# Performance work log

Hardware: AMD Instinct MI355X
Metric: run time of the kernel (lower is better)

The kernel has to match this reference:

```python
import jax, jax.numpy as jnp
import numpy as np

NU, NI, E = 20000, 8000, 64
DV, DT = 4096, 768
NE, B = 200000, 4096
L_HET, L_HOMO = 2, 1
K_ISG, K_UCG = 10, 20
MMW, WD = 0.1, 1e-4


def setup_inputs() -> dict:
    ks = jax.random.split(jax.random.key(0), 14)
    return {
        "feat_v": jax.random.normal(ks[0], (NI, DV), jnp.float32),
        "feat_t": jax.random.normal(ks[1], (NI, DT), jnp.float32),
        "pref_v": jax.random.normal(ks[2], (NU, E), jnp.float32) * 0.1,
        "pref_t": jax.random.normal(ks[3], (NU, E), jnp.float32) * 0.1,
        "W_v": jax.random.normal(ks[4], (DV, E), jnp.float32) * 0.02,
        "W_t": jax.random.normal(ks[5], (DT, E), jnp.float32) * 0.02,
        "user_v_alpha": jax.random.normal(ks[6], (1,), jnp.float32),
        "user_nb_weights": jax.random.normal(ks[7], (NU, K_UCG), jnp.float32),
        "edge_users": jax.random.randint(ks[8], (NE,), 0, NU, jnp.int32),
        "edge_items": jax.random.randint(ks[9], (NE,), 0, NI, jnp.int32),
        "u_ids": jax.random.randint(ks[10], (B,), 0, NU, jnp.int32),
        "pos_ids": jax.random.randint(ks[11], (B,), 0, NI, jnp.int32),
        "neg_ids": jax.random.randint(ks[12], (B,), 0, NI, jnp.int32),
        "user_nb": jax.random.randint(ks[13], (NU, K_UCG), 0, NU, jnp.int32),
    }


def reference(feat_v, feat_t, pref_v, pref_t, W_v, W_t, user_v_alpha,
              user_nb_weights, edge_users, edge_items, u_ids, pos_ids,
              neg_ids, user_nb):
    N = NU + NI
    # bidirectional bipartite edges (items offset by NU)
    src = jnp.concatenate([edge_users, edge_items + NU])
    dst = jnp.concatenate([edge_items + NU, edge_users])
    deg = jax.ops.segment_sum(jnp.ones_like(src, jnp.float32), dst, num_segments=N)
    deg = jnp.maximum(deg, 1.0)
    norm = (1.0 / jnp.sqrt(deg[src] * deg[dst]))[:, None]

    def hetero_gcn(feat, pref, W):
        x = jnp.concatenate([pref, feat @ W], axis=0)  # [N, E]
        h, out = x, x
        for _ in range(L_HET):
            h = jax.ops.segment_sum(h[src] * norm, dst, num_segments=N)
            out = out + h
        return out[:NU], out[NU:]

    u_v, i_v = hetero_gcn(feat_v, pref_v, W_v)
    u_t, i_t = hetero_gcn(feat_t, pref_t, W_t)
    a_v = jax.nn.sigmoid(user_v_alpha[0])
    u_f = jnp.concatenate([a_v * u_v, (1.0 - a_v) * u_t], axis=1)  # [NU, 2E]
    i_f = jnp.concatenate([i_v, i_t], axis=1)                      # [NI, 2E]

    # Item Semantic Graph: KNN over cosine sim, no grad through adjacency.
    def knn_adj(f):
        fn = f / jnp.linalg.norm(f, axis=-1, keepdims=True)
        sim = fn @ fn.T                       # [NI, NI]
        _, idx = jax.lax.top_k(sim, K_ISG)
        return jnp.zeros((NI, NI), f.dtype).at[jnp.arange(NI)[:, None], idx].set(1.0)

    adj = jax.lax.stop_gradient(MMW * knn_adj(feat_v) + (1.0 - MMW) * knn_adj(feat_t))
    rs = adj.sum(axis=1)
    adj = adj * jnp.where(rs > 0, 1.0 / rs, 0.0)[:, None]

    h_i = i_f
    for _ in range(L_HOMO):
        h_i = adj @ h_i

    # User Co-occurrence Graph: scatter-softmax attention aggregation, vectorized.
    attn = jax.nn.softmax(user_nb_weights, axis=1)  # [NU, K]
    h_u = u_f
    for _ in range(L_HOMO):
        h_u = jnp.einsum('uk,ukd->ud', attn, h_u[user_nb])

    z_u = u_f + h_u
    z_i = i_f + h_i
    pos = jnp.sum(z_u[u_ids] * z_i[pos_ids], axis=1)
    neg = jnp.sum(z_u[u_ids] * z_i[neg_ids], axis=1)
    bpr = -jnp.mean(jax.nn.log_sigmoid(pos - neg))
    reg = WD * (jnp.sum(pref_v ** 2) + jnp.sum(pref_t ** 2) + user_v_alpha[0] ** 2) / 2.0
    return bpr + reg
```

## Files before the change

kernel.cpp:

```cpp
#include <hip/hip_runtime.h>
#include <cstdint>
#include <cstddef>

#define NU_C   20000
#define NI_C   8000
#define NTOT_C 28000
#define NE_C   200000
#define B_C    4096
#define NPAD_C 8064
#define NCHUNK 63
#define NPAIR  2016
#define NEB    782

typedef unsigned short u16;
typedef unsigned int   u32;
typedef unsigned char  u8;
typedef __bf16 bf16x8 __attribute__((ext_vector_type(8)));
typedef float  f32x4  __attribute__((ext_vector_type(4)));

static __device__ __forceinline__ u16 f2bf(float f) {
  u32 u = __float_as_uint(f);
  return (u16)((u + 0x7fffu + ((u >> 16) & 1u)) >> 16);
}

static __device__ __forceinline__ void gl_lds16(const void* g, void* l) {
  __builtin_amdgcn_global_load_lds(
      (const __attribute__((address_space(1))) void*)g,
      (__attribute__((address_space(3))) void*)l, 16, 0, 0);
}

static __device__ __forceinline__ int xcd_swz(int b) {
  return (b & 7) * (NPAIR / 8) + (b >> 3);
}

static __device__ __forceinline__ void wtrans_body(int b, const float* __restrict__ Wv,
                                                   const float* __restrict__ Wti,
                                                   u16* __restrict__ Ov, u16* __restrict__ Ot) {
  __shared__ u16 sT[64][72];
  const float* W; u16* O; int D;
  if (b < 64) { W = Wv; O = Ov; D = 4096; }
  else        { b -= 64; W = Wti; O = Ot; D = 768; }
  const int k0 = b * 64;
  const int r = threadIdx.x >> 6;
  const int c = threadIdx.x & 63;
  for (int rr = r; rr < 64; rr += 4)
    sT[c][rr] = f2bf(W[(size_t)(k0 + rr) * 64 + c]);
  __syncthreads();
  const int n = threadIdx.x >> 2, seg = threadIdx.x & 3;
  uint4 a0 = *(const uint4*)&sT[n][seg * 16];
  uint4 a1 = *(const uint4*)&sT[n][seg * 16 + 8];
  *(uint4*)(O + (size_t)n * D + k0 + seg * 16)     = a0;
  *(uint4*)(O + (size_t)n * D + k0 + seg * 16 + 8) = a1;
}

__global__ void conv_kernel2(const float* __restrict__ Fv, const float* __restrict__ Ft,
                             u16* __restrict__ Fbv, u16* __restrict__ Fbt,
                             u8* __restrict__ Fv8,
                             float* __restrict__ rnv, float* __restrict__ rnt,
                             const float* __restrict__ pv, const float* __restrict__ pt,
                             float* __restrict__ x2,
                             const float* __restrict__ Wv, const float* __restrict__ Wti,
                             u16* __restrict__ wtv, u16* __restrict__ wtt,
                             const int* __restrict__ eu, const int* __restrict__ ei,
                             float* __restrict__ deg,
                             const float* __restrict__ alpha, float* __restrict__ out) {
  int b = blockIdx.x;
  const int tid = threadIdx.x;
  float ss = 0.f;
  if (b < NPAD_C) {
    const int row = b;
    u16* dst  = Fbv + (size_t)row * 4096;
    u8*  dst8 = Fv8 + (size_t)row * 4096;
    if (row < NI_C) {
      const float* src = Fv + (size_t)row * 4096;
      for (int c = tid * 4; c < 4096; c += 1024) {
        float4 f = *(const float4*)(src + c);
        ss += f.x*f.x + f.y*f.y + f.z*f.z + f.w*f.w;
        ushort4 v; v.x = f2bf(f.x); v.y = f2bf(f.y); v.z = f2bf(f.z); v.w = f2bf(f.w);
        *(ushort4*)(dst + c) = v;
        int w8 = __builtin_amdgcn_cvt_pk_fp8_f32(f.x, f.y, 0, false);
        w8 = __builtin_amdgcn_cvt_pk_fp8_f32(f.z, f.w, w8, true);
        *(u32*)(dst8 + c) = (u32)w8;
      }
    } else {
      for (int c = tid * 4; c < 4096; c += 1024) {
        ushort4 v; v.x = v.y = v.z = v.w = 0;
        *(ushort4*)(dst + c) = v;
        *(u32*)(dst8 + c) = 0u;
      }
    }
    #pragma unroll
    for (int off = 32; off; off >>= 1) ss += __shfl_xor(ss, off);
    __shared__ float red[4];
    if ((tid & 63) == 0) red[tid >> 6] = ss;
    __syncthreads();
    if (tid == 0) {
      float s = red[0] + red[1] + red[2] + red[3];
      rnv[row] = (row < NI_C) ? rsqrtf(s) : 0.f;
    }
  } else if (b < 2 * NPAD_C) {
    const int row = b - NPAD_C;
    u16* dst = Fbt + (size_t)row * 768;
    if (row < NI_C) {
      const float* src = Ft + (size_t)row * 768;
      for (int c = tid * 4; c < 768; c += 1024) {
        float4 f = *(const float4*)(src + c);
        ss += f.x*f.x + f.y*f.y + f.z*f.z + f.w*f.w;
        ushort4 v; v.x = f2bf(f.x); v.y = f2bf(f.y); v.z = f2bf(f.z); v.w = f2bf(f.w);
        *(ushort4*)(dst + c) = v;
      }
    } else {
      for (int c = tid * 4; c < 768; c += 1024) {
        ushort4 v; v.x = v.y = v.z = v.w = 0;
        *(ushort4*)(dst + c) = v;
      }
    }
    #pragma unroll
    for (int off = 32; off; off >>= 1) ss += __shfl_xor(ss, off);
    __shared__ float red[4];
    if ((tid & 63) == 0) red[tid >> 6] = ss;
    __syncthreads();
    if (tid == 0) {
      float s = red[0] + red[1] + red[2] + red[3];
      rnt[row] = (row < NI_C) ? rsqrtf(s) : 0.f;
    }
  } else if (b < 2 * NPAD_C + 76) {
    wtrans_body(b - 2 * NPAD_C, Wv, Wti, wtv, wtt);
  } else if (b < 2 * NPAD_C + 76 + 1250) {
    const int b2 = b - (2 * NPAD_C + 76);
    #pragma unroll
    for (int k = 0; k < 8; ++k) {
      int gid = b2 * 2048 + k * 256 + tid;
      int u = gid >> 7, c = gid & 127;
      x2[gid] = (c < 64) ? pv[(size_t)u * 64 + c] : pt[(size_t)u * 64 + (c - 64)];
    }
  } else if (b < 2 * NPAD_C + 76 + 1250 + NEB) {
    const int b2 = b - (2 * NPAD_C + 76 + 1250);
    int e = b2 * 256 + tid;
    if (e < NE_C) {
      atomicAdd(&deg[eu[e]], 1.f);
      atomicAdd(&deg[NU_C + ei[e]], 1.f);
    }
  } else {
    const int b2 = b - (2 * NPAD_C + 76 + 1250 + NEB);
    const size_t N1 = (size_t)NU_C * 64;
    float acc = 0.f;
    for (size_t i = (size_t)b2 * 256 + tid; i < 2 * N1; i += (size_t)512 * 256) {
      float x = (i < N1) ? pv[i] : pt[i - N1];
      acc += x * x;
    }
    #pragma unroll
    for (int off = 32; off; off >>= 1) acc += __shfl_xor(acc, off);
    __shared__ float red2[4];
    if ((tid & 63) == 0) red2[tid >> 6] = acc;
    __syncthreads();
    if (tid == 0) {
      float s = red2[0] + red2[1] + red2[2] + red2[3];
      atomicAdd(out, 0.5e-4f * s);
    }
    if (b2 == 0 && tid == 0) {
      float a = alpha[0];
      atomicAdd(out, 0.5e-4f * a * a);
    }
  }
}

static __device__ __forceinline__ void simtopk_fp8_body(
    int bid, char* smem, const u8* __restrict__ F, const float* __restrict__ rn,
    u32* __restrict__ tv) {
  u8*    sB   = (u8*)smem;
  u8*    sA   = (u8*)(smem + 16384);
  float* T    = (float*)smem;
  int*   mk   = (int*)smem;
  int*   mk2  = (int*)(smem + 20480);
  float* sRNI = (float*)(smem + 33792);
  float* sRNJ = (float*)(smem + 34304);

  const int tid  = threadIdx.x;
  const int lane = tid & 63;
  const int wv   = tid >> 6;
  const int n15  = lane & 15;
  const int quad = lane >> 4;

  int I = 0, rem = xcd_swz(bid);
  { int rowlen = NCHUNK;
    while (rem >= rowlen) { rem -= rowlen; rowlen--; I++; } }
  const int J = I + rem;

  const int l2   = lane >> 2;
  const int lseg = (lane & 3) ^ (l2 & 3) ^ (lane >> 4);
  const u8* gB[2]; const u8* gA[2]; u8* lB[2]; u8* lA[2];
  #pragma unroll
  for (int rep = 0; rep < 2; ++rep) {
    int row = wv * 32 + rep * 16 + l2;
    gB[rep] = F + (size_t)(I * 128 + row) * 4096 + lseg * 16;
    gA[rep] = F + (size_t)(J * 128 + row) * 4096 + lseg * 16;
    lB[rep] = sB + (wv * 32 + rep * 16) * 64;
    lA[rep] = sA + (wv * 32 + rep * 16) * 64;
  }
  const int s_n = (n15 & 3) ^ (n15 >> 2);
  const int q2  = quad >> 1;
  const int q8  = (quad & 1) * 8;
  const int rB0 = (wv * 32 + n15) * 64;
  const int rB1 = rB0 + 16 * 64;

  f32x4 acc[2][8];
  #pragma unroll
  for (int tf = 0; tf < 2; ++tf)
    #pragma unroll
    for (int af = 0; af < 8; ++af) { f32x4 z = {0.f,0.f,0.f,0.f}; acc[tf][af] = z; }

  for (int k0 = 0; k0 < 4096; k0 += 128) {
    __syncthreads();
    gl_lds16(gB[0] + k0,      lB[0]);
    gl_lds16(gB[0] + k0 + 64, lB[0] + 8192);
    gl_lds16(gB[1] + k0,      lB[1]);
    gl_lds16(gB[1] + k0 + 64, lB[1] + 8192);
    gl_lds16(gA[0] + k0,      lA[0]);
    gl_lds16(gA[0] + k0 + 64, lA[0] + 8192);
    gl_lds16(gA[1] + k0,      lA[1]);
    gl_lds16(gA[1] + k0 + 64, lA[1] + 8192);
    if (k0 == 0) {
      if (tid < 128) sRNJ[tid] = rn[J * 128 + tid];
      else           sRNI[tid - 128] = rn[I * 128 + (tid - 128)];
    }
    __syncthreads();
    #pragma unroll
    for (int ksub = 0; ksub < 2; ++ksub) {
      const u8* bBase = sB + ksub * 8192;
      const u8* aBase = sA + ksub * 8192;
      #pragma unroll
      for (int ks = 0; ks < 2; ++ks) {
        const int sw = (((ks * 2 + q2) ^ s_n) << 4) + q8;
        long long b0 = *(const long long*)(bBase + rB0 + sw);
        long long b1 = *(const long long*)(bBase + rB1 + sw);
        #pragma unroll
        for (int af = 0; af < 8; ++af) {
          long long a = *(const long long*)(aBase + (af * 16 + n15) * 64 + sw);
          acc[0][af] = __builtin_amdgcn_mfma_f32_16x16x32_fp8_fp8(a, b0, acc[0][af], 0, 0, 0);
          acc[1][af] = __builtin_amdgcn_mfma_f32_16x16x32_fp8_fp8(a, b1, acc[1][af], 0, 0, 0);
        }
      }
    }
  }

  int bk[2][10];
  #pragma unroll
  for (int tf = 0; tf < 2; ++tf)
    #pragma unroll
    for (int j = 0; j < 10; ++j) bk[tf][j] = 0;

  #pragma unroll
  for (int af = 0; af < 8; ++af) {
    const float4 rn4 = *(const float4*)(sRNJ + af * 16 + quad * 4);
    const float rna[4] = {rn4.x, rn4.y, rn4.z, rn4.w};
    #pragma unroll
    for (int r = 0; r < 4; ++r) {
      const int ci = J * 128 + af * 16 + quad * 4 + r;
      #pragma unroll
      for (int tf = 0; tf < 2; ++tf) {
        float v = acc[tf][af][r] * rna[r];
        int key = (int)((__float_as_uint(v) & 0xFFFFE000u) | (u32)ci);
        if (ci < NI_C && key > bk[tf][9]) {
          bk[tf][9] = key;
          #pragma unroll
          for (int j = 9; j > 0; --j)
            if (bk[tf][j] > bk[tf][j-1]) { int t = bk[tf][j]; bk[tf][j] = bk[tf][j-1]; bk[tf][j-1] = t; }
        }
      }
    }
  }
  __syncthreads();
  #pragma unroll
  for (int tf = 0; tf < 2; ++tf) {
    int rl = wv * 32 + tf * 16 + n15;
    #pragma unroll
    for (int j = 0; j < 10; ++j) mk[rl * 40 + quad * 10 + j] = bk[tf][j];
  }
  __syncthreads();
  if (tid < 128) {
    int* m = mk + tid * 40;
    int h0 = 0, h1 = 10, h2 = 20, h3 = 30;
    int v0 = m[0], v1 = m[10], v2 = m[20], v3 = m[30];
    #pragma unroll
    for (int s = 0; s < 10; ++s) {
      int m01 = v0 > v1 ? v0 : v1, m23 = v2 > v3 ? v2 : v3;
      int mx = m01 > m23 ? m01 : m23;
      mk2[tid * 10 + s] = mx;
      if      (mx == v0) { ++h0; v0 = (h0 < 10) ? m[h0] : (int)0x80000000; }
      else if (mx == v1) { ++h1; v1 = (h1 < 20) ? m[h1] : (int)0x80000000; }
      else if (mx == v2) { ++h2; v2 = (h2 < 30) ? m[h2] : (int)0x80000000; }
      else               { ++h3; v3 = (h3 < 40) ? m[h3] : (int)0x80000000; }
    }
  }
  __syncthreads();
  { u32* o = tv + ((size_t)J * NPAD_C + I * 128) * 10;
    for (int g = tid; g < 1280; g += 256) o[g] = (u32)mk2[g]; }

  if (I == J) return;

  int bj[2][10];
  #pragma unroll
  for (int s = 0; s < 2; ++s)
    #pragma unroll
    for (int j = 0; j < 10; ++j) bj[s][j] = 0;

  #pragma unroll
  for (int tf = 0; tf < 2; ++tf) {
    __syncthreads();
    #pragma unroll
    for (int af = 0; af < 8; ++af)
      #pragma unroll
      for (int r = 0; r < 4; ++r)
        T[(af * 16 + quad * 4 + r) * 66 + wv * 16 + n15] = acc[tf][af][r];
    __syncthreads();
    #pragma unroll
    for (int s = 0; s < 2; ++s) {
      const int c_own = wv * 32 + s * 16 + n15;
      #pragma unroll
      for (int j = 0; j < 16; ++j) {
        const int t  = quad * 32 + tf * 16 + j;
        const int t64 = quad * 16 + j;
        float v = T[c_own * 66 + t64] * sRNI[t];
        const int ti = I * 128 + t;
        int key = (int)((__float_as_uint(v) & 0xFFFFE000u) | (u32)ti);
        if (ti < NI_C && key > bj[s][9]) {
          bj[s][9] = key;
          #pragma unroll
          for (int q = 9; q > 0; --q)
            if (bj[s][q] > bj[s][q-1]) { int tt = bj[s][q]; bj[s][q] = bj[s][q-1]; bj[s][q-1] = tt; }
        }
      }
    }
  }
  __syncthreads();
  #pragma unroll
  for (int s = 0; s < 2; ++s) {
    int rl = wv * 32 + s * 16 + n15;
    #pragma unroll
    for (int j = 0; j < 10; ++j) mk[rl * 40 + quad * 10 + j] = bj[s][j];
  }
  __syncthreads();
  if (tid < 128) {
    int* m = mk + tid * 40;
    int h0 = 0, h1 = 10, h2 = 20, h3 = 30;
    int v0 = m[0], v1 = m[10], v2 = m[20], v3 = m[30];
    #pragma unroll
    for (int s = 0; s < 10; ++s) {
      int m01 = v0 > v1 ? v0 : v1, m23 = v2 > v3 ? v2 : v3;
      int mx = m01 > m23 ? m01 : m23;
      mk2[tid * 10 + s] = mx;
      if      (mx == v0) { ++h0; v0 = (h0 < 10) ? m[h0] : (int)0x80000000; }
      else if (mx == v1) { ++h1; v1 = (h1 < 20) ? m[h1] : (int)0x80000000; }
      else if (mx == v2) { ++h2; v2 = (h2 < 30) ? m[h2] : (int)0x80000000; }
      else               { ++h3; v3 = (h3 < 40) ? m[h3] : (int)0x80000000; }
    }
  }
  __syncthreads();
  { u32* o = tv + ((size_t)I * NPAD_C + J * 128) * 10;
    for (int g = tid; g < 1280; g += 256) o[g] = (u32)mk2[g]; }
}

static __device__ __forceinline__ void simtopk_bf16_body(
    int bid, char* smem, const u16* __restrict__ F, const float* __restrict__ rn,
    u32* __restrict__ tv) {
  u16*   sB   = (u16*)smem;
  u16*   sA   = (u16*)(smem + 16384);
  float* T    = (float*)smem;
  int*   mk   = (int*)smem;
  int*   mk2  = (int*)(smem + 20480);
  float* sRNI = (float*)(smem + 34816);
  float* sRNJ = (float*)(smem + 35328);

  const int tid  = threadIdx.x;
  const int lane = tid & 63;
  const int wv   = tid >> 6;
  const int n15  = lane & 15;
  const int quad = lane >> 4;

  int I = 0, rem = xcd_swz(bid);
  { int rowlen = NCHUNK;
    while (rem >= rowlen) { rem -= rowlen; rowlen--; I++; } }
  const int J = I + rem;

  const int l8  = lane >> 3;
  const int sgu = ((lane & 7) ^ l8) << 3;
  const u16* gB[4]; const u16* gA[4]; u16* lB[4]; u16* lA[4];
  #pragma unroll
  for (int rep = 0; rep < 4; ++rep) {
    int row = wv * 32 + rep * 8 + l8;
    gB[rep] = F + (size_t)(I * 128 + row) * 768 + sgu;
    gA[rep] = F + (size_t)(J * 128 + row) * 768 + sgu;
    lB[rep] = sB + wv * 2048 + rep * 512;
    lA[rep] = sA + wv * 2048 + rep * 512;
  }
  const int swu0 = ((quad    ) ^ (n15 & 7)) << 3;
  const int swu1 = ((quad + 4) ^ (n15 & 7)) << 3;
  const int rowB0 = (wv * 32 + n15) * 64;
  const int rowB1 = rowB0 + 16 * 64;

  f32x4 acc[2][8];
  #pragma unroll
  for (int tf = 0; tf < 2; ++tf)
    #pragma unroll
    for (int af = 0; af < 8; ++af) { f32x4 z = {0.f,0.f,0.f,0.f}; acc[tf][af] = z; }

  for (int k0 = 0; k0 < 768; k0 += 64) {
    __syncthreads();
    #pragma unroll
    for (int rep = 0; rep < 4; ++rep) gl_lds16(gB[rep] + k0, lB[rep]);
    #pragma unroll
    for (int rep = 0; rep < 4; ++rep) gl_lds16(gA[rep] + k0, lA[rep]);
    if (k0 == 0) {
      if (tid < 128) sRNJ[tid] = rn[J * 128 + tid];
      else           sRNI[tid - 128] = rn[I * 128 + (tid - 128)];
    }
    __syncthreads();
    #pragma unroll
    for (int ks = 0; ks < 2; ++ks) {
      const int swu = ks ? swu1 : swu0;
      bf16x8 b0 = *(const bf16x8*)(sB + rowB0 + swu);
      bf16x8 b1 = *(const bf16x8*)(sB + rowB1 + swu);
      #pragma unroll
      for (int af = 0; af < 8; ++af) {
        bf16x8 a = *(const bf16x8*)(sA + (af * 16 + n15) * 64 + swu);
        acc[0][af] = __builtin_amdgcn_mfma_f32_16x16x32_bf16(a, b0, acc[0][af], 0, 0, 0);
        acc[1][af] = __builtin_amdgcn_mfma_f32_16x16x32_bf16(a, b1, acc[1][af], 0, 0, 0);
      }
    }
  }

  int bk[2][10];
  #pragma unroll
  for (int tf = 0; tf < 2; ++tf)
    #pragma unroll
    for (int j = 0; j < 10; ++j) bk[tf][j] = 0;

  #pragma unroll
  for (int af = 0; af < 8; ++af) {
    const float4 rn4 = *(const float4*)(sRNJ + af * 16 + quad * 4);
    const float rna[4] = {rn4.x, rn4.y, rn4.z, rn4.w};
    #pragma unroll
    for (int r = 0; r < 4; ++r) {
      const int ci = J * 128 + af * 16 + quad * 4 + r;
      #pragma unroll
      for (int tf = 0; tf < 2; ++tf) {
        float v = acc[tf][af][r] * rna[r];
        int key = (int)((__float_as_uint(v) & 0xFFFFE000u) | (u32)ci);
        if (ci < NI_C && key > bk[tf][9]) {
          bk[tf][9] = key;
          #pragma unroll
          for (int j = 9; j > 0; --j)
            if (bk[tf][j] > bk[tf][j-1]) { int t = bk[tf][j]; bk[tf][j] = bk[tf][j-1]; bk[tf][j-1] = t; }
        }
      }
    }
  }
  __syncthreads();
  #pragma unroll
  for (int tf = 0; tf < 2; ++tf) {
    int rl = wv * 32 + tf * 16 + n15;
    #pragma unroll
    for (int j = 0; j < 10; ++j) mk[rl * 40 + quad * 10 + j] = bk[tf][j];
  }
  __syncthreads();
  if (tid < 128) {
    int* m = mk + tid * 40;
    int h0 = 0, h1 = 10, h2 = 20, h3 = 30;
    int v0 = m[0], v1 = m[10], v2 = m[20], v3 = m[30];
    #pragma unroll
    for (int s = 0; s < 10; ++s) {
      int m01 = v0 > v1 ? v0 : v1, m23 = v2 > v3 ? v2 : v3;
      int mx = m01 > m23 ? m01 : m23;
      mk2[tid * 10 + s] = mx;
      if      (mx == v0) { ++h0; v0 = (h0 < 10) ? m[h0] : (int)0x80000000; }
      else if (mx == v1) { ++h1; v1 = (h1 < 20) ? m[h1] : (int)0x80000000; }
      else if (mx == v2) { ++h2; v2 = (h2 < 30) ? m[h2] : (int)0x80000000; }
      else               { ++h3; v3 = (h3 < 40) ? m[h3] : (int)0x80000000; }
    }
  }
  __syncthreads();
  { u32* o = tv + ((size_t)J * NPAD_C + I * 128) * 10;
    for (int g = tid; g < 1280; g += 256) o[g] = (u32)mk2[g]; }

  if (I == J) return;

  int bj[2][10];
  #pragma unroll
  for (int s = 0; s < 2; ++s)
    #pragma unroll
    for (int j = 0; j < 10; ++j) bj[s][j] = 0;

  #pragma unroll
  for (int tf = 0; tf < 2; ++tf) {
    __syncthreads();
    #pragma unroll
    for (int af = 0; af < 8; ++af)
      #pragma unroll
      for (int r = 0; r < 4; ++r)
        T[(af * 16 + quad * 4 + r) * 66 + wv * 16 + n15] = acc[tf][af][r];
    __syncthreads();
    #pragma unroll
    for (int s = 0; s < 2; ++s) {
      const int c_own = wv * 32 + s * 16 + n15;
      #pragma unroll
      for (int j = 0; j < 16; ++j) {
        const int t  = quad * 32 + tf * 16 + j;
        const int t64 = quad * 16 + j;
        float v = T[c_own * 66 + t64] * sRNI[t];
        const int ti = I * 128 + t;
        int key = (int)((__float_as_uint(v) & 0xFFFFE000u) | (u32)ti);
        if (ti < NI_C && key > bj[s][9]) {
          bj[s][9] = key;
          #pragma unroll
          for (int q = 9; q > 0; --q)
            if (bj[s][q] > bj[s][q-1]) { int tt = bj[s][q]; bj[s][q] = bj[s][q-1]; bj[s][q-1] = tt; }
        }
      }
    }
  }
  __syncthreads();
  #pragma unroll
  for (int s = 0; s < 2; ++s) {
    int rl = wv * 32 + s * 16 + n15;
    #pragma unroll
    for (int j = 0; j < 10; ++j) mk[rl * 40 + quad * 10 + j] = bj[s][j];
  }
  __syncthreads();
  if (tid < 128) {
    int* m = mk + tid * 40;
    int h0 = 0, h1 = 10, h2 = 20, h3 = 30;
    int v0 = m[0], v1 = m[10], v2 = m[20], v3 = m[30];
    #pragma unroll
    for (int s = 0; s < 10; ++s) {
      int m01 = v0 > v1 ? v0 : v1, m23 = v2 > v3 ? v2 : v3;
      int mx = m01 > m23 ? m01 : m23;
      mk2[tid * 10 + s] = mx;
      if      (mx == v0) { ++h0; v0 = (h0 < 10) ? m[h0] : (int)0x80000000; }
      else if (mx == v1) { ++h1; v1 = (h1 < 20) ? m[h1] : (int)0x80000000; }
      else if (mx == v2) { ++h2; v2 = (h2 < 30) ? m[h2] : (int)0x80000000; }
      else               { ++h3; v3 = (h3 < 40) ? m[h3] : (int)0x80000000; }
    }
  }
  __syncthreads();
  { u32* o = tv + ((size_t)I * NPAD_C + J * 128) * 10;
    for (int g = tid; g < 1280; g += 256) o[g] = (u32)mk2[g]; }
}

static __device__ __forceinline__ void merge4_body(int mb, int* fkbase,
                                                   const u32* __restrict__ tv,
                                                   int* __restrict__ idx) {
  const int w    = threadIdx.x >> 6;
  const int lane = threadIdx.x & 63;
  const int row  = mb * 4 + w;
  int* fk = fkbase + w * 640;
  for (int g = lane; g < 630; g += 64)
    fk[g] = (int)tv[((size_t)(g / 10) * NPAD_C + row) * 10 + (g % 10)];
  if (lane < 10) fk[630 + lane] = (int)0x80000000;
  __syncthreads();
  int v[10];
  #pragma unroll
  for (int j = 0; j < 10; ++j) v[j] = fk[lane + j * 64];
  #pragma unroll 1
  for (int s = 0; s < 10; ++s) {
    int loc = v[0];
    #pragma unroll
    for (int j = 1; j < 10; ++j) loc = v[j] > loc ? v[j] : loc;
    #pragma unroll
    for (int off = 32; off; off >>= 1) {
      int o = __shfl_xor(loc, off); loc = o > loc ? o : loc;
    }
    if (lane == 0) idx[row * 10 + s] = loc & 0x1FFF;
    #pragma unroll
    for (int j = 0; j < 10; ++j) if (v[j] == loc) v[j] = (int)0x80000000;
  }
}

template<int D>
static __device__ __forceinline__ void gemm_xw_body(
    int bid, char* smem, const u16* __restrict__ F, const u16* __restrict__ Wt,
    float* __restrict__ x2, int modeoff) {
  u16* sF = (u16*)smem;
  const int tid  = threadIdx.x;
  const int lane = tid & 63;
  const int wv   = tid >> 6;
  const int n15  = lane & 15;
  const int quad = lane >> 4;
  const int l8   = lane >> 3;
  const int sgu  = ((lane & 7) ^ l8) << 3;
  const u16* gF[2]; u16* lF[2];
  #pragma unroll
  for (int rep = 0; rep < 2; ++rep) {
    int row = rep * 32 + wv * 8 + l8;
    gF[rep] = F + (size_t)(bid * 64 + row) * D + sgu;
    lF[rep] = sF + (rep * 32 + wv * 8) * 64;
  }
  const int swu0 = ((quad    ) ^ (n15 & 7)) << 3;
  const int swu1 = ((quad + 4) ^ (n15 & 7)) << 3;

  f32x4 acc[4];
  #pragma unroll
  for (int nf = 0; nf < 4; ++nf) { f32x4 z = {0.f,0.f,0.f,0.f}; acc[nf] = z; }

  for (int k0 = 0; k0 < D; k0 += 64) {
    __syncthreads();
    gl_lds16(gF[0] + k0, lF[0]);
    gl_lds16(gF[1] + k0, lF[1]);
    __syncthreads();
    #pragma unroll
    for (int ks = 0; ks < 2; ++ks) {
      const int swu = ks ? swu1 : swu0;
      bf16x8 a = *(const bf16x8*)(sF + (wv * 16 + n15) * 64 + swu);
      #pragma unroll
      for (int nf = 0; nf < 4; ++nf) {
        bf16x8 b = *(const bf16x8*)(Wt + (size_t)(nf * 16 + n15) * D + k0 + ks * 32 + quad * 8);
        acc[nf] = __builtin_amdgcn_mfma_f32_16x16x32_bf16(a, b, acc[nf], 0, 0, 0);
      }
    }
  }
  #pragma unroll
  for (int nf = 0; nf < 4; ++nf)
    #pragma unroll
    for (int r = 0; r < 4; ++r) {
      int row = bid * 64 + wv * 16 + quad * 4 + r;
      if (row < NI_C)
        x2[(size_t)(NU_C + row) * 128 + modeoff + nf * 16 + n15] = acc[nf][r];
    }
}

static __device__ __forceinline__ void gather2_body(
    int bid, const int* __restrict__ row_start, const int* __restrict__ esrc,
    const float* __restrict__ ew, const float* __restrict__ x2, float* __restrict__ h1) {
  const int node = bid * 2 + (threadIdx.x >> 7);
  const int ch   = threadIdx.x & 127;
  if (node >= NTOT_C) return;
  const int b = row_start[node], e = row_start[node + 1];
  float acc = 0.f;
  for (int i = b; i < e; ++i)
    acc += ew[i] * x2[(size_t)esrc[i] * 128 + ch];
  h1[(size_t)node * 128 + ch] = acc;
}

static __device__ __forceinline__ void gather_comb2_body(
    int bid, const int* __restrict__ row_start, const int* __restrict__ esrc,
    const float* __restrict__ ew, const float* __restrict__ x2,
    const float* __restrict__ h1, const float* __restrict__ alpha,
    float* __restrict__ uf, float* __restrict__ ifb) {
  const int node = bid * 2 + (threadIdx.x >> 7);
  const int ch   = threadIdx.x & 127;
  if (node >= NTOT_C) return;
  const int b = row_start[node], e = row_start[node + 1];
  float acc = 0.f;
  for (int i = b; i < e; ++i)
    acc += ew[i] * h1[(size_t)esrc[i] * 128 + ch];
  float val = x2[(size_t)node * 128 + ch] + h1[(size_t)node * 128 + ch] + acc;
  if (node < NU_C) {
    float av = 1.f / (1.f + expf(-alpha[0]));
    float coef = (ch < 64) ? av : (1.f - av);
    uf[(size_t)node * 128 + ch] = coef * val;
  } else {
    ifb[(size_t)(node - NU_C) * 128 + ch] = val;
  }
}

static __device__ __forceinline__ void place_body(
    int bid, const int* __restrict__ eu, const int* __restrict__ ei,
    const float* __restrict__ dinv, int* __restrict__ cursor,
    int* __restrict__ esrc, float* __restrict__ ew) {
  int e = bid * 256 + threadIdx.x;
  if (e >= NE_C) return;
  int u = eu[e], v = NU_C + ei[e];
  float w = dinv[u] * dinv[v];
  int p1 = atomicAdd(&cursor[v], 1);  esrc[p1] = u; ew[p1] = w;
  int p2 = atomicAdd(&cursor[u], 1);  esrc[p2] = v; ew[p2] = w;
}

__launch_bounds__(256)
__global__ void fusedA_kernel(const u8* __restrict__ F8, const float* __restrict__ rnv,
                              u32* __restrict__ tv,
                              const u16* __restrict__ Fvb, const u16* __restrict__ Wtv,
                              const u16* __restrict__ Ftb, const u16* __restrict__ Wtt,
                              float* __restrict__ x2,
                              const int* __restrict__ eu, const int* __restrict__ ei,
                              const float* __restrict__ dinv, int* __restrict__ cursor,
                              int* __restrict__ esrc, float* __restrict__ ew) {
  __shared__ __align__(16) char smem[34816];
  int b = blockIdx.x;
  if (b < 125) { gemm_xw_body<4096>(b, smem, Fvb, Wtv, x2, 0); return; }
  b -= 125;
  if (b < 125) { gemm_xw_body<768>(b, smem, Ftb, Wtt, x2, 64); return; }
  b -= 125;
  if (b < NPAIR) { simtopk_fp8_body(b, smem, F8, rnv, tv); return; }
  place_body(b - NPAIR, eu, ei, dinv, cursor, esrc, ew);
}

__launch_bounds__(256)
__global__ void fusedB_kernel(const u16* __restrict__ Ftb, const float* __restrict__ rnt,
                              u32* __restrict__ tv2,
                              const u32* __restrict__ tv, int* __restrict__ idx,
                              const int* __restrict__ row_start, const int* __restrict__ esrc,
                              const float* __restrict__ ew, const float* __restrict__ x2,
                              float* __restrict__ h1) {
  __shared__ __align__(16) char smem[40960];
  int b = blockIdx.x;
  if (b < NPAIR) { simtopk_bf16_body(b, smem, Ftb, rnt, tv2); return; }
  b -= NPAIR;
  if (b < 2000) { merge4_body(b, (int*)smem, tv, idx); return; }
  gather2_body(b - 2000, row_start, esrc, ew, x2, h1);
}

__launch_bounds__(256)
__global__ void fusedC_kernel(const u32* __restrict__ tv2, int* __restrict__ idxt,
                              const int* __restrict__ row_start, const int* __restrict__ esrc,
                              const float* __restrict__ ew, const float* __restrict__ x2,
                              const float* __restrict__ h1, const float* __restrict__ alpha,
                              float* __restrict__ uf, float* __restrict__ ifb) {
  __shared__ __align__(16) int fk[4 * 640];
  int b = blockIdx.x;
  if (b < 2000) { merge4_body(b, fk, tv2, idxt); return; }
  gather_comb2_body(b - 2000, row_start, esrc, ew, x2, h1, alpha, uf, ifb);
}

__global__ void scan_kernel(float* __restrict__ deg, int* __restrict__ row_start,
                            int* __restrict__ cursor) {
  __shared__ int part[1024];
  const int tid = threadIdx.x;
  const int base = tid * 28;
  float dl[28];
  int local[28];
  int s = 0;
  #pragma unroll
  for (int j = 0; j < 28; ++j) {
    int n = base + j;
    float df = (n < NTOT_C) ? deg[n] : 0.f;
    dl[j] = df;
    local[j] = s; s += (int)df;
  }
  part[tid] = s;
  __syncthreads();
  for (int off = 1; off < 1024; off <<= 1) {
    int v = (tid >= off) ? part[tid - off] : 0;
    __syncthreads();
    part[tid] += v;
    __syncthreads();
  }
  int pre = (tid > 0) ? part[tid - 1] : 0;
  #pragma unroll
  for (int j = 0; j < 28; ++j) {
    int n = base + j;
    if (n < NTOT_C) {
      row_start[n] = pre + local[j];
      cursor[n]    = pre + local[j];
      deg[n]       = rsqrtf(fmaxf(dl[j], 1.f));
    }
  }
  if (tid == 1023) row_start[NTOT_C] = part[1023];
}

__launch_bounds__(256)
__global__ void zuloss_kernel(const float* __restrict__ uf, const float* __restrict__ w,
                              const int* __restrict__ nb, const float* __restrict__ ifb,
                              const int* __restrict__ iv, const int* __restrict__ it,
                              const int* __restrict__ uid, const int* __restrict__ pid,
                              const int* __restrict__ nid, float* __restrict__ out) {
  const int wv = threadIdx.x >> 6, lane = threadIdx.x & 63;
  const int b = blockIdx.x * 4 + wv;
  const int u = uid[b], p = pid[b], n = nid[b];
  const int c = lane * 2;

  float e[20]; float m = -1e30f;
  #pragma unroll
  for (int k = 0; k < 20; ++k) { e[k] = w[u * 20 + k]; m = fmaxf(m, e[k]); }
  float ssum = 0.f;
  #pragma unroll
  for (int k = 0; k < 20; ++k) { e[k] = expf(e[k] - m); ssum += e[k]; }
  float inv = 1.f / ssum;

  float2 zu = *(const float2*)(uf + (size_t)u * 128 + c);
  float ax = 0.f, ay = 0.f;
  #pragma unroll
  for (int k = 0; k < 20; ++k) {
    int j = nb[u * 20 + k];
    float2 t = *(const float2*)(uf + (size_t)j * 128 + c);
    ax += e[k] * inv * t.x;
    ay += e[k] * inv * t.y;
  }
  zu.x += ax; zu.y += ay;

  float2 zp, zn;
  #pragma unroll
  for (int side = 0; side < 2; ++side) {
    const int i = side ? n : p;
    float svx = 0.f, svy = 0.f, stx = 0.f, sty = 0.f;
    #pragma unroll
    for (int k = 0; k < 10; ++k) {
      float2 t = *(const float2*)(ifb + (size_t)iv[i * 10 + k] * 128 + c);
      svx += t.x; svy += t.y;
    }
    #pragma unroll
    for (int k = 0; k < 10; ++k) {
      float2 t = *(const float2*)(ifb + (size_t)it[i * 10 + k] * 128 + c);
      stx += t.x; sty += t.y;
    }
    float2 base = *(const float2*)(ifb + (size_t)i * 128 + c);
    float2 r;
    r.x = base.x + 0.01f * svx + 0.09f * stx;
    r.y = base.y + 0.01f * svy + 0.09f * sty;
    if (side) zn = r; else zp = r;
  }

  float d = zu.x * (zp.x - zn.x) + zu.y * (zp.y - zn.y);
  #pragma unroll
  for (int off = 32; off; off >>= 1) d += __shfl_xor(d, off);
  if (lane == 0) {
    float xv = -d;
    float sp = fmaxf(xv, 0.f) + log1pf(expf(-fabsf(xv)));
    atomicAdd(out, sp * (1.f / (float)B_C));
  }
}

extern "C" void kernel_launch(void* const* d_in, const int* in_sizes, int n_in,
                              void* d_out, int out_size, void* d_ws, size_t ws_size,
                              hipStream_t stream) {
  const float* feat_v = (const float*)d_in[0];
  const float* feat_t = (const float*)d_in[1];
  const float* pref_v = (const float*)d_in[2];
  const float* pref_t = (const float*)d_in[3];
  const float* W_v    = (const float*)d_in[4];
  const float* W_t    = (const float*)d_in[5];
  const float* alpha  = (const float*)d_in[6];
  const float* unw    = (const float*)d_in[7];
  const int* eu       = (const int*)d_in[8];
  const int* ei       = (const int*)d_in[9];
  const int* u_ids    = (const int*)d_in[10];
  const int* pos_ids  = (const int*)d_in[11];
  const int* neg_ids  = (const int*)d_in[12];
  const int* user_nb  = (const int*)d_in[13];
  float* out = (float*)d_out;
  char* ws = (char*)d_ws;

  size_t off = 0;
  auto alloc = [&](size_t bytes) { char* p = ws + off; off += (bytes + 255) & ~(size_t)255; return p; };
  u16*   fvbf  = (u16*)alloc((size_t)NPAD_C * 4096 * 2);
  u8*    fv8   = (u8*)alloc((size_t)NPAD_C * 4096);
  u16*   ftbf  = (u16*)alloc((size_t)NPAD_C * 768 * 2);
  u16*   wtv   = (u16*)alloc((size_t)64 * 4096 * 2);
  u16*   wtt   = (u16*)alloc((size_t)64 * 768 * 2);
  float* rn_v  = (float*)alloc(NPAD_C * 4);
  float* rn_t  = (float*)alloc(NPAD_C * 4);
  int*   idx_v = (int*)alloc(NI_C * 10 * 4);
  int*   idx_t = (int*)alloc(NI_C * 10 * 4);
  float* dinv  = (float*)alloc(NTOT_C * 4);
  int*   rowst = (int*)alloc((NTOT_C + 1) * 4);
  int*   curs  = (int*)alloc(NTOT_C * 4);
  int*   esrc  = (int*)alloc((size_t)2 * NE_C * 4);
  float* ew    = (float*)alloc((size_t)2 * NE_C * 4);
  float* x2    = (float*)alloc((size_t)NTOT_C * 128 * 4);
  float* h1    = (float*)alloc((size_t)NTOT_C * 128 * 4);
  char*  pC    = alloc((size_t)(NU_C + NI_C) * 128 * 4);
  u32*   tvb   = (u32*)pC;
  char*  pC2   = alloc((size_t)6 * 1024 * 1024 + 256);
  (void)pC2;
  u32*   tvb2  = (u32*)fvbf;
  float* u_f   = (float*)pC;
  float* i_f   = (float*)(pC + (size_t)NU_C * 128 * 4);

  hipMemsetAsync(out, 0, sizeof(float), stream);
  hipMemsetAsync(dinv, 0, NTOT_C * 4, stream);

  conv_kernel2<<<2 * NPAD_C + 76 + 1250 + NEB + 512, 256, 0, stream>>>(
      feat_v, feat_t, fvbf, ftbf, fv8, rn_v, rn_t, pref_v, pref_t, x2,
      W_v, W_t, wtv, wtt, eu, ei, dinv, alpha, out);

  scan_kernel<<<1, 1024, 0, stream>>>(dinv, rowst, curs);

  fusedA_kernel<<<250 + NPAIR + NEB, 256, 0, stream>>>(
      fv8, rn_v, tvb, fvbf, wtv, ftbf, wtt, x2, eu, ei, dinv, curs, esrc, ew);

  fusedB_kernel<<<NPAIR + 2000 + 14000, 256, 0, stream>>>(
      ftbf, rn_t, tvb2, tvb, idx_v, rowst, esrc, ew, x2, h1);

  fusedC_kernel<<<2000 + 14000, 256, 0, stream>>>(
      tvb2, idx_t, rowst, esrc, ew, x2, h1, alpha, u_f, i_f);

  zuloss_kernel<<<1024, 256, 0, stream>>>(u_f, unw, user_nb, i_f, idx_v, idx_t,
                                          u_ids, pos_ids, neg_ids, out);
}
```

Baseline: 986.0 us.

## Split fused B/C kernels to shrink LDS and rebalance gather/merge phases

Splits the bf16 sim-topk plus merge work away from the first GCN gather, pairs that gather with the text top-k merge, and gives the final gather-combine its own launch. The sim-topk scratch layout is packed tighter so the kernel needs 34816 bytes of LDS instead of 40960, which may allow more resident blocks per CU. The zuloss softmax over 20 neighbour weights now uses wave shuffles instead of per-lane serial loads and exps. The cost is one extra kernel launch and a different overlap pattern between the memory-bound gathers and the compute-heavy top-k.

```diff
diff --git a/kernel.cpp b/kernel.cpp
--- a/kernel.cpp
+++ b/kernel.cpp
@@ -369,8 +369,8 @@
   float* T    = (float*)smem;
   int*   mk   = (int*)smem;
   int*   mk2  = (int*)(smem + 20480);
-  float* sRNI = (float*)(smem + 34816);
-  float* sRNJ = (float*)(smem + 35328);
+  float* sRNI = (float*)(smem + 33792);
+  float* sRNJ = (float*)(smem + 34304);
 
   const int tid  = threadIdx.x;
   const int lane = tid & 63;
@@ -695,30 +695,32 @@
 }
 
 __launch_bounds__(256)
-__global__ void fusedB_kernel(const u16* __restrict__ Ftb, const float* __restrict__ rnt,
-                              u32* __restrict__ tv2,
-                              const u32* __restrict__ tv, int* __restrict__ idx,
-                              const int* __restrict__ row_start, const int* __restrict__ esrc,
-                              const float* __restrict__ ew, const float* __restrict__ x2,
-                              float* __restrict__ h1) {
-  __shared__ __align__(16) char smem[40960];
+__global__ void fusedB1_kernel(const u16* __restrict__ Ftb, const float* __restrict__ rnt,
+                               u32* __restrict__ tv2,
+                               const u32* __restrict__ tv, int* __restrict__ idx) {
+  __shared__ __align__(16) char smem[34816];
   int b = blockIdx.x;
   if (b < NPAIR) { simtopk_bf16_body(b, smem, Ftb, rnt, tv2); return; }
-  b -= NPAIR;
-  if (b < 2000) { merge4_body(b, (int*)smem, tv, idx); return; }
-  gather2_body(b - 2000, row_start, esrc, ew, x2, h1);
+  merge4_body(b - NPAIR, (int*)smem, tv, idx);
 }
 
 __launch_bounds__(256)
-__global__ void fusedC_kernel(const u32* __restrict__ tv2, int* __restrict__ idxt,
-                              const int* __restrict__ row_start, const int* __restrict__ esrc,
-                              const float* __restrict__ ew, const float* __restrict__ x2,
-                              const float* __restrict__ h1, const float* __restrict__ alpha,
-                              float* __restrict__ uf, float* __restrict__ ifb) {
+__global__ void fusedB2_kernel(const int* __restrict__ row_start, const int* __restrict__ esrc,
+                               const float* __restrict__ ew, const float* __restrict__ x2,
+                               float* __restrict__ h1,
+                               const u32* __restrict__ tv2, int* __restrict__ idxt) {
   __shared__ __align__(16) int fk[4 * 640];
   int b = blockIdx.x;
-  if (b < 2000) { merge4_body(b, fk, tv2, idxt); return; }
-  gather_comb2_body(b - 2000, row_start, esrc, ew, x2, h1, alpha, uf, ifb);
+  if (b < 14000) { gather2_body(b, row_start, esrc, ew, x2, h1); return; }
+  merge4_body(b - 14000, fk, tv2, idxt);
+}
+
+__launch_bounds__(256)
+__global__ void gcomb_kernel(const int* __restrict__ row_start, const int* __restrict__ esrc,
+                             const float* __restrict__ ew, const float* __restrict__ x2,
+                             const float* __restrict__ h1, const float* __restrict__ alpha,
+                             float* __restrict__ uf, float* __restrict__ ifb) {
+  gather_comb2_body(blockIdx.x, row_start, esrc, ew, x2, h1, alpha, uf, ifb);
 }
 
 __global__ void scan_kernel(float* __restrict__ deg, int* __restrict__ row_start,
@@ -768,12 +770,14 @@
   const int u = uid[b], p = pid[b], n = nid[b];
   const int c = lane * 2;
 
-  float e[20]; float m = -1e30f;
-  #pragma unroll
-  for (int k = 0; k < 20; ++k) { e[k] = w[u * 20 + k]; m = fmaxf(m, e[k]); }
-  float ssum = 0.f;
-  #pragma unroll
-  for (int k = 0; k < 20; ++k) { e[k] = expf(e[k] - m); ssum += e[k]; }
+  float mv = (lane < 20) ? w[u * 20 + lane] : -1e30f;
+  float m = mv;
+  #pragma unroll
+  for (int off = 32; off; off >>= 1) m = fmaxf(m, __shfl_xor(m, off));
+  float ek_own = expf(mv - m);
+  float e[20]; float ssum = 0.f;
+  #pragma unroll
+  for (int k = 0; k < 20; ++k) { e[k] = __shfl(ek_own, k); ssum += e[k]; }
   float inv = 1.f / ssum;
 
   float2 zu = *(const float2*)(uf + (size_t)u * 128 + c);
@@ -877,11 +881,11 @@
   fusedA_kernel<<<250 + NPAIR + NEB, 256, 0, stream>>>(
       fv8, rn_v, tvb, fvbf, wtv, ftbf, wtt, x2, eu, ei, dinv, curs, esrc, ew);
 
-  fusedB_kernel<<<NPAIR + 2000 + 14000, 256, 0, stream>>>(
-      ftbf, rn_t, tvb2, tvb, idx_v, rowst, esrc, ew, x2, h1);
-
-  fusedC_kernel<<<2000 + 14000, 256, 0, stream>>>(
-      tvb2, idx_t, rowst, esrc, ew, x2, h1, alpha, u_f, i_f);
+  fusedB1_kernel<<<NPAIR + 2000, 256, 0, stream>>>(ftbf, rn_t, tvb2, tvb, idx_v);
+
+  fusedB2_kernel<<<14000 + 2000, 256, 0, stream>>>(rowst, esrc, ew, x2, h1, tvb2, idx_t);
+
+  gcomb_kernel<<<14000, 256, 0, stream>>>(rowst, esrc, ew, x2, h1, alpha, u_f, i_f);
 
   zuloss_kernel<<<1024, 256, 0, stream>>>(u_f, unw, user_nb, i_f, idx_v, idx_t,
                                           u_ids, pos_ids, neg_ids, out);
```

Measured after the change: 906.9 us. 8.0% less time.
